# Performance work log

Hardware: AMD Instinct MI355X
Metric: run time of the kernel (lower is better)

## Reference

```python
import jax, jax.numpy as jnp
import numpy as np

B, T, D = 8, 2048, 512
KQ, K = 32, 4  # DemandRouter defaults: k_query=32, k_topk=4


def setup_inputs() -> dict:
    key = jax.random.key(0)
    ks = jax.random.split(key, 9)

    def init(k, shape, fan_in):
        return (jax.random.normal(k, shape, jnp.float32) / np.sqrt(fan_in)).astype(jnp.float32)

    return dict(
        x=jax.random.normal(ks[0], (B, T, D), jnp.float32),
        # DemandRouter projections
        Wq=init(ks[1], (D, KQ), D), bq=jnp.zeros((KQ,), jnp.float32),
        Wk=init(ks[2], (D, KQ), D), bk=jnp.zeros((KQ,), jnp.float32),
        # System1 FFN (D -> 2D -> D) + LayerNorm
        W1=init(ks[3], (D, 2 * D), D), b1=jnp.zeros((2 * D,), jnp.float32),
        W2=init(ks[4], (2 * D, D), 2 * D), b2=jnp.zeros((D,), jnp.float32),
        ln_g=jnp.ones((D,), jnp.float32), ln_b=jnp.zeros((D,), jnp.float32),
        # System2 transform (2D -> 2D -> D)
        Wt1=init(ks[5], (2 * D, 2 * D), 2 * D), bt1=jnp.zeros((2 * D,), jnp.float32),
        Wt2=init(ks[6], (2 * D, D), 2 * D), bt2=jnp.zeros((D,), jnp.float32),
        # output projection
        Wo=init(ks[7], (D, D), D), bo=jnp.zeros((D,), jnp.float32),
    )


def reference(x, Wq, bq, Wk, bk, W1, b1, W2, b2, ln_g, ln_b, Wt1, bt1, Wt2, bt2, Wo, bo):
    # ---- DemandRouter: topk over query-key similarity, gather neighbors, mean ----
    q = x @ Wq + bq                      # [B,T,KQ]
    k = x @ Wk + bk                      # [B,T,KQ]
    sim = jnp.einsum('btk,bsk->bts', q, k) / np.float32(np.sqrt(KQ))  # [B,T,T]
    _, idx = jax.lax.top_k(sim, K)       # [B,T,K]
    # gather x[b, idx[b,t]] and mean over K neighbors -> [B,T,D]
    gathered = jax.vmap(lambda xb, ib: xb[ib])(x, idx).mean(axis=2)

    # ---- System1: residual FFN (exact GELU) + LayerNorm ----
    h = jax.nn.gelu(gathered @ W1 + b1, approximate=False) @ W2 + b2
    y = gathered + h
    mu = y.mean(-1, keepdims=True)
    var = y.var(-1, keepdims=True)
    y = (y - mu) / jnp.sqrt(var + 1e-5) * ln_g + ln_b  # [B,T,D]

    # ---- System2: sequential gated memory update over T ----
    def step(mem, xt):  # mem: [B,D], xt: [B,D]
        e = jnp.concatenate([xt, mem], axis=-1)                       # [B,2D]
        prop = jax.nn.gelu(e @ Wt1 + bt1, approximate=False) @ Wt2 + bt2  # [B,D]
        g = jax.nn.sigmoid(prop)
        mem = mem * (1.0 - g) + prop * g
        return mem, None

    mem0 = jnp.zeros((y.shape[0], y.shape[2]), y.dtype)
    mem_final, _ = jax.lax.scan(step, mem0, jnp.swapaxes(y, 0, 1))

    # pooled = system2_out[:, -1] == final memory
    return mem_final @ Wo + bo  # [B,D]
```

## Files before the change

kernel.cpp:

```cpp
#include <hip/hip_runtime.h>
#include <math.h>
#include <stdint.h>


using bf16x8 = __attribute__((ext_vector_type(8))) short;
using f32x4v = __attribute__((ext_vector_type(4))) float;
typedef unsigned long long ull;

__device__ inline unsigned short f2b(float f) {
  union { float f; unsigned int u; } v; v.f = f;
  unsigned int r = v.u + 0x7fffu + ((v.u >> 16) & 1u);
  return (unsigned short)(r >> 16);
}

__device__ inline float gelu_f(float x) {
  return 0.5f * x * (1.0f + erff(x * 0.70710678118654752f));
}

__device__ inline void ins4(float v, int i,
                            float& v0, int& i0, float& v1, int& i1,
                            float& v2, int& i2, float& v3, int& i3) {
  bool b0 = (v > v0) || (v == v0 && i < i0);
  bool b1 = (v > v1) || (v == v1 && i < i1);
  bool b2 = (v > v2) || (v == v2 && i < i2);
  bool b3 = (v > v3) || (v == v3 && i < i3);
  float nv3 = b2 ? v2 : (b3 ? v : v3); int ni3 = b2 ? i2 : (b3 ? i : i3);
  float nv2 = b1 ? v1 : (b2 ? v : v2); int ni2 = b1 ? i1 : (b2 ? i : i2);
  float nv1 = b0 ? v0 : (b1 ? v : v1); int ni1 = b0 ? i0 : (b1 ? i : i1);
  float nv0 = b0 ? v  : v0;            int ni0 = b0 ? i  : i0;
  v0=nv0; i0=ni0; v1=nv1; i1=ni1; v2=nv2; i2=ni2; v3=nv3; i3=ni3;
}


__global__ __launch_bounds__(256)
void wqk_kernel(const float* __restrict__ Wq, const float* __restrict__ Wk,
                float* __restrict__ wqk) {
  int id = blockIdx.x * 256 + threadIdx.x;
  int d = id >> 6, c = id & 63;
  wqk[id] = (c < 32) ? Wq[d * 32 + c] : Wk[d * 32 + (c - 32)];
}

__global__ __launch_bounds__(256)
void transpose_bf16_kernel(const float* __restrict__ src,
                           unsigned short* __restrict__ dst, int K, int N) {
  __shared__ float tile[32][33];
  int bk = blockIdx.x << 5, bn = blockIdx.y << 5;
  int c = threadIdx.x & 31, r8 = threadIdx.x >> 5;
  for (int r = r8; r < 32; r += 8) tile[r][c] = src[(size_t)(bk + r) * N + bn + c];
  __syncthreads();
  for (int r = r8; r < 32; r += 8) dst[(size_t)(bn + r) * K + bk + c] = f2b(tile[c][r]);
}

__global__ __launch_bounds__(256)
void transpose_f32_kernel(const float* __restrict__ src,
                          float* __restrict__ dst, int K, int N) {
  __shared__ float tile[32][33];
  int bk = blockIdx.x << 5, bn = blockIdx.y << 5;
  int c = threadIdx.x & 31, r8 = threadIdx.x >> 5;
  for (int r = r8; r < 32; r += 8) tile[r][c] = src[(size_t)(bk + r) * N + bn + c];
  __syncthreads();
  for (int r = r8; r < 32; r += 8) dst[(size_t)(bn + r) * K + bk + c] = tile[c][r];
}


__global__ __launch_bounds__(256)
void qk_kernel(const float* __restrict__ x, const float* __restrict__ wqk,
               const float* __restrict__ bq, const float* __restrict__ bk,
               float* __restrict__ qkout) {
  __shared__ float xs[16][512];
  int tid = threadIdx.x;
  int b = blockIdx.x >> 7;
  int t0 = (blockIdx.x & 127) << 4;
  const float* xb = x + ((size_t)(b * 2048 + t0)) * 512;
#pragma unroll
  for (int i = 0; i < 8; ++i) {
    int f = i * 256 + tid;
    int r = f >> 7, c4 = f & 127;
    *(float4*)&xs[r][c4 * 4] = *(const float4*)&xb[(size_t)r * 512 + c4 * 4];
  }
  __syncthreads();
  int c = tid & 63, r4 = tid >> 6;
  float a0 = 0.f, a1 = 0.f, a2 = 0.f, a3 = 0.f;
#pragma unroll 4
  for (int d = 0; d < 512; ++d) {
    float w = wqk[d * 64 + c];
    a0 += xs[r4][d] * w;
    a1 += xs[r4 + 4][d] * w;
    a2 += xs[r4 + 8][d] * w;
    a3 += xs[r4 + 12][d] * w;
  }
  float bias = (c < 32) ? bq[c] : bk[c - 32];
  size_t base = ((size_t)(b * 2048 + t0)) * 64 + c;
  qkout[base + (size_t)r4 * 64] = a0 + bias;
  qkout[base + (size_t)(r4 + 4) * 64] = a1 + bias;
  qkout[base + (size_t)(r4 + 8) * 64] = a2 + bias;
  qkout[base + (size_t)(r4 + 12) * 64] = a3 + bias;
}

__global__ __launch_bounds__(256)
void topk_kernel(const float* __restrict__ qkb, int* __restrict__ idxout) {
  __shared__ float qs[16][36];
  __shared__ float ks[128][36];
  __shared__ float mv[16][16][4];
  __shared__ int   mi[16][16][4];
  int tid = threadIdx.x;
  int b = blockIdx.x >> 7;
  int t0 = (blockIdx.x & 127) << 4;
  const float* qb = qkb + ((size_t)b * 2048) * 64;
  if (tid < 128) {
    int r = tid >> 3, c4 = tid & 7;
    *(float4*)&qs[r][c4 * 4] = *(const float4*)&qb[(size_t)(t0 + r) * 64 + c4 * 4];
  }
  __syncthreads();
  int tl = tid >> 4, sl = tid & 15;
  float qv[32];
#pragma unroll
  for (int kk = 0; kk < 32; ++kk) qv[kk] = qs[tl][kk];
  float v0 = -INFINITY, v1 = -INFINITY, v2 = -INFINITY, v3 = -INFINITY;
  int i0 = 0x7fffffff, i1 = 0x7fffffff, i2 = 0x7fffffff, i3 = 0x7fffffff;
  for (int s0 = 0; s0 < 2048; s0 += 128) {
    __syncthreads();
#pragma unroll
    for (int p = 0; p < 4; ++p) {
      int f = p * 256 + tid;
      int r = f >> 3, c4 = f & 7;
      *(float4*)&ks[r][c4 * 4] =
          *(const float4*)&qb[(size_t)(s0 + r) * 64 + 32 + c4 * 4];
    }
    __syncthreads();
#pragma unroll
    for (int j = 0; j < 8; ++j) {
      int srow = j * 16 + sl;
      float accv = 0.f;
#pragma unroll
      for (int k4 = 0; k4 < 8; ++k4) {
        float4 kv = *(const float4*)&ks[srow][k4 * 4];
        accv += qv[k4 * 4 + 0] * kv.x + qv[k4 * 4 + 1] * kv.y +
                qv[k4 * 4 + 2] * kv.z + qv[k4 * 4 + 3] * kv.w;
      }
      ins4(accv, s0 + srow, v0, i0, v1, i1, v2, i2, v3, i3);
    }
  }
  mv[tl][sl][0] = v0; mv[tl][sl][1] = v1; mv[tl][sl][2] = v2; mv[tl][sl][3] = v3;
  mi[tl][sl][0] = i0; mi[tl][sl][1] = i1; mi[tl][sl][2] = i2; mi[tl][sl][3] = i3;
  __syncthreads();
  if (tid < 16) {
    float w0 = -INFINITY, w1 = -INFINITY, w2 = -INFINITY, w3 = -INFINITY;
    int a0 = 0x7fffffff, a1 = 0x7fffffff, a2 = 0x7fffffff, a3 = 0x7fffffff;
    for (int ss = 0; ss < 16; ++ss)
#pragma unroll
      for (int q = 0; q < 4; ++q)
        ins4(mv[tid][ss][q], mi[tid][ss][q], w0, a0, w1, a1, w2, a2, w3, a3);
    int4 o; o.x = a0; o.y = a1; o.z = a2; o.w = a3;
    *(int4*)&idxout[((size_t)(b * 2048 + t0 + tid)) * 4] = o;
  }
}

__global__ __launch_bounds__(128)
void gather_kernel(const float* __restrict__ x, const int* __restrict__ idx,
                   float* __restrict__ gf, unsigned short* __restrict__ gb) {
  int bt = blockIdx.x;
  int b = bt >> 11;
  const int4 iv = *(const int4*)&idx[(size_t)bt * 4];
  int tid = threadIdx.x;
  const float* xb = x + ((size_t)b * 2048) * 512;
  float4 p0 = *(const float4*)&xb[(size_t)iv.x * 512 + tid * 4];
  float4 p1 = *(const float4*)&xb[(size_t)iv.y * 512 + tid * 4];
  float4 p2 = *(const float4*)&xb[(size_t)iv.z * 512 + tid * 4];
  float4 p3 = *(const float4*)&xb[(size_t)iv.w * 512 + tid * 4];
  float4 m;
  m.x = (p0.x + p1.x + p2.x + p3.x) * 0.25f;
  m.y = (p0.y + p1.y + p2.y + p3.y) * 0.25f;
  m.z = (p0.z + p1.z + p2.z + p3.z) * 0.25f;
  m.w = (p0.w + p1.w + p2.w + p3.w) * 0.25f;
  *(float4*)&gf[(size_t)bt * 512 + tid * 4] = m;
  ushort4 u; u.x = f2b(m.x); u.y = f2b(m.y); u.z = f2b(m.z); u.w = f2b(m.w);
  *(ushort4*)&gb[(size_t)bt * 512 + tid * 4] = u;
}


template <int MODE>
__global__ __launch_bounds__(256, 2)
void gemm_bf16_k(const unsigned short* __restrict__ A,
                 const unsigned short* __restrict__ Bt,
                 const float* __restrict__ bias,
                 const float* __restrict__ resid,
                 void* __restrict__ outp, int M, int N, int K) {
  __shared__ unsigned short sA[128 * 32];
  __shared__ unsigned short sB[128 * 32];
  const int tid = threadIdx.x;
  const int lane = tid & 63, wave = tid >> 6;
  const int m0 = blockIdx.x * 128, n0 = blockIdx.y * 128;
  const int col16 = lane & 15, quad = lane >> 4;
  const int wm = wave >> 1, wn = wave & 1;
  f32x4v acc[4][4];
#pragma unroll
  for (int i = 0; i < 4; ++i)
#pragma unroll
    for (int j = 0; j < 4; ++j) {
      f32x4v z = {0.f, 0.f, 0.f, 0.f};
      acc[i][j] = z;
    }
  const int nkt = K >> 5;
  for (int kt = 0; kt < nkt; ++kt) {
    const int k0 = kt << 5;
#pragma unroll
    for (int p = 0; p < 2; ++p) {
      int f = p * 256 + tid;
      int row = f >> 2, q4 = f & 3;
      *(uint4*)&sA[row * 32 + q4 * 8] =
          *(const uint4*)(A + (size_t)(m0 + row) * K + k0 + q4 * 8);
      *(uint4*)&sB[row * 32 + q4 * 8] =
          *(const uint4*)(Bt + (size_t)(n0 + row) * K + k0 + q4 * 8);
    }
    __syncthreads();
    bf16x8 af[4], bfr[4];
#pragma unroll
    for (int i = 0; i < 4; ++i)
      af[i] = *(const bf16x8*)&sA[(wm * 64 + i * 16 + col16) * 32 + quad * 8];
#pragma unroll
    for (int j = 0; j < 4; ++j)
      bfr[j] = *(const bf16x8*)&sB[(wn * 64 + j * 16 + col16) * 32 + quad * 8];
#pragma unroll
    for (int i = 0; i < 4; ++i)
#pragma unroll
      for (int j = 0; j < 4; ++j)
        acc[i][j] = __builtin_amdgcn_mfma_f32_16x16x32_bf16(af[i], bfr[j],
                                                            acc[i][j], 0, 0, 0);
    __syncthreads();
  }
  float* outf = (float*)outp;
  unsigned short* outb = (unsigned short*)outp;
#pragma unroll
  for (int i = 0; i < 4; ++i)
#pragma unroll
    for (int j = 0; j < 4; ++j) {
      int col = n0 + wn * 64 + j * 16 + col16;
      float bs = bias[col];
#pragma unroll
      for (int r = 0; r < 4; ++r) {
        int row = m0 + wm * 64 + i * 16 + quad * 4 + r;
        float v = acc[i][j][r] + bs;
        if (MODE == 0) {
          outb[(size_t)row * N + col] = f2b(gelu_f(v));
        } else if (MODE == 1) {
          outf[(size_t)row * N + col] = v + resid[(size_t)row * N + col];
        } else {
          outf[(size_t)row * N + col] = v;
        }
      }
    }
}


__global__ __launch_bounds__(128)
void ln_kernel(const float* __restrict__ ypre, const float* __restrict__ lg,
               const float* __restrict__ lb, unsigned short* __restrict__ yb) {
  int row = blockIdx.x, tid = threadIdx.x;
  float4 v = *(const float4*)&ypre[(size_t)row * 512 + tid * 4];
  float s = v.x + v.y + v.z + v.w;
  float sq = v.x * v.x + v.y * v.y + v.z * v.z + v.w * v.w;
#pragma unroll
  for (int off = 1; off < 64; off <<= 1) {
    s += __shfl_xor(s, off, 64);
    sq += __shfl_xor(sq, off, 64);
  }
  __shared__ float red[4];
  if ((tid & 63) == 0) { red[(tid >> 6) * 2] = s; red[(tid >> 6) * 2 + 1] = sq; }
  __syncthreads();
  float S = red[0] + red[2], SQ = red[1] + red[3];
  float mu = S * (1.f / 512.f);
  float var = SQ * (1.f / 512.f) - mu * mu;
  float rstd = rsqrtf(var + 1e-5f);
  float4 g4 = *(const float4*)&lg[tid * 4];
  float4 b4 = *(const float4*)&lb[tid * 4];
  ushort4 u;
  u.x = f2b((v.x - mu) * rstd * g4.x + b4.x);
  u.y = f2b((v.y - mu) * rstd * g4.y + b4.y);
  u.z = f2b((v.z - mu) * rstd * g4.z + b4.z);
  u.w = f2b((v.w - mu) * rstd * g4.w + b4.w);
  *(ushort4*)&yb[(size_t)row * 512 + tid * 4] = u;
}


__global__ __launch_bounds__(256)
void system2_kernel(const float* __restrict__ Wt1, const float* __restrict__ Wt2T,
                    const float* __restrict__ bt2, const float* __restrict__ xpart,
                    ull* __restrict__ guT, ull* __restrict__ memT,
                    float* __restrict__ memfinal) {
  __shared__ float WbT[32 * 516];
  __shared__ float W2S[16 * 1028];
  __shared__ float memS[512];
  __shared__ float guA[1024];
  __shared__ float parts1[256];
  __shared__ float red2[256];

  const int t = threadIdx.x;
  const int team = blockIdx.x & 7;
  const int g = blockIdx.x >> 3;
  const int ucol0 = g << 5;
  const int mcol0 = g << 4;

  for (int idx = t; idx < 32 * 512; idx += 256) {
    int j = idx & 31, k = idx >> 5;
    WbT[j * 516 + k] = Wt1[(size_t)(512 + k) * 1024 + ucol0 + j];
  }
  for (int idx = t; idx < 16 * 1024; idx += 256) {
    int dd = idx >> 10, u = idx & 1023;
    W2S[dd * 1028 + u] = Wt2T[(size_t)(mcol0 + dd) * 1024 + u];
  }
  memS[t] = 0.f;
  memS[t + 256] = 0.f;
  const float bt2r = (t < 16) ? bt2[mcol0 + t] : 0.f;
  __syncthreads();

  const int j = t & 31, c = t >> 5;
  const int dd = t & 15, c2 = t >> 4;
  const float* xp = xpart + (size_t)team * 2048 * 1024 + ucol0;
  float xv = (t < 32) ? xp[t] : 0.f;

  for (int s = 0; s < 2048; ++s) {
    const int par = s & 1;
    ull* gub = guT + (size_t)(par * 8 + team) * 1024;
    ull* memb = memT + (size_t)(par * 8 + team) * 512;
    const unsigned utag = (unsigned)(s + 1);
    const ull tagw = ((ull)utag) << 32;

    float xnext = (t < 32 && s < 2047) ? xp[(size_t)(s + 1) * 1024 + t] : 0.f;

    {
      const float* wrow = &WbT[j * 516 + c * 64];
      const float* mrow = &memS[c * 64];
      float p1 = 0.f;
#pragma unroll
      for (int i = 0; i < 64; i += 4) {
        float4 wv = *(const float4*)&wrow[i];
        float4 mv = *(const float4*)&mrow[i];
        p1 += wv.x * mv.x + wv.y * mv.y + wv.z * mv.z + wv.w * mv.w;
      }
      parts1[c * 32 + j] = p1;
    }
    __syncthreads();
    if (t < 32) {
      float u = xv;
#pragma unroll
      for (int cc = 0; cc < 8; ++cc) u += parts1[cc * 32 + t];
      float gv = gelu_f(u);
      union { float f; unsigned u; } uv; uv.f = gv;
      __hip_atomic_store(&gub[ucol0 + t], tagw | uv.u, __ATOMIC_RELAXED,
                         __HIP_MEMORY_SCOPE_AGENT);
    }
    asm volatile("" ::: "memory");

    {
      ull* p = &gub[t * 4];
      ull v0, v1, v2, v3;
      for (;;) {
        v0 = __hip_atomic_load(&p[0], __ATOMIC_RELAXED, __HIP_MEMORY_SCOPE_AGENT);
        v1 = __hip_atomic_load(&p[1], __ATOMIC_RELAXED, __HIP_MEMORY_SCOPE_AGENT);
        v2 = __hip_atomic_load(&p[2], __ATOMIC_RELAXED, __HIP_MEMORY_SCOPE_AGENT);
        v3 = __hip_atomic_load(&p[3], __ATOMIC_RELAXED, __HIP_MEMORY_SCOPE_AGENT);
        bool ok = ((unsigned)(v0 >> 32) == utag) & ((unsigned)(v1 >> 32) == utag) &
                  ((unsigned)(v2 >> 32) == utag) & ((unsigned)(v3 >> 32) == utag);
        if (ok) break;
        __builtin_amdgcn_s_sleep(1);
      }
      union { unsigned u; float f; } a0, a1, a2, a3;
      a0.u = (unsigned)v0; a1.u = (unsigned)v1;
      a2.u = (unsigned)v2; a3.u = (unsigned)v3;
      guA[t * 4 + 0] = a0.f;
      guA[t * 4 + 1] = a1.f;
      guA[t * 4 + 2] = a2.f;
      guA[t * 4 + 3] = a3.f;
    }
    __syncthreads();

    {
      const float* wrow = &W2S[dd * 1028 + c2 * 64];
      const float* grow = &guA[c2 * 64];
      float p2 = 0.f;
#pragma unroll
      for (int i = 0; i < 64; i += 4) {
        float4 wv = *(const float4*)&wrow[i];
        float4 gv = *(const float4*)&grow[i];
        p2 += wv.x * gv.x + wv.y * gv.y + wv.z * gv.z + wv.w * gv.w;
      }
      red2[c2 * 16 + dd] = p2;
    }
    __syncthreads();
    if (t < 16) {
      float prop = bt2r;
#pragma unroll
      for (int cc = 0; cc < 16; ++cc) prop += red2[cc * 16 + t];
      float gate = 1.f / (1.f + __expf(-prop));
      float mnew = memS[mcol0 + t] * (1.f - gate) + prop * gate;
      union { float f; unsigned u; } mv; mv.f = mnew;
      __hip_atomic_store(&memb[mcol0 + t], tagw | mv.u, __ATOMIC_RELAXED,
                         __HIP_MEMORY_SCOPE_AGENT);
    }
    asm volatile("" ::: "memory");

    {
      ull* q1 = &memb[t * 2];
      ull* q2 = &memb[t * 2 + 1];
      ull v1, v2;
      for (;;) {
        v1 = __hip_atomic_load(q1, __ATOMIC_RELAXED, __HIP_MEMORY_SCOPE_AGENT);
        v2 = __hip_atomic_load(q2, __ATOMIC_RELAXED, __HIP_MEMORY_SCOPE_AGENT);
        if ((unsigned)(v1 >> 32) == utag && (unsigned)(v2 >> 32) == utag) break;
        __builtin_amdgcn_s_sleep(1);
      }
      union { unsigned u; float f; } m1, m2;
      m1.u = (unsigned)v1; m2.u = (unsigned)v2;
      memS[t * 2] = m1.f;
      memS[t * 2 + 1] = m2.f;
    }
    xv = xnext;
    __syncthreads();
  }

  if (g == 0 && t < 128)
    *(float4*)&memfinal[(size_t)team * 512 + t * 4] = *(float4*)&memS[t * 4];
}


__global__ __launch_bounds__(256)
void out_gemv_kernel(const float* __restrict__ memf, const float* __restrict__ Wo,
                     const float* __restrict__ bo, float* __restrict__ out) {
  int gid = blockIdx.x * 256 + threadIdx.x;
  int b = gid >> 9, d = gid & 511;
  const float* mb = memf + (size_t)b * 512;
  float acc = bo[d];
#pragma unroll 8
  for (int k = 0; k < 512; ++k) acc += mb[k] * Wo[(size_t)k * 512 + d];
  out[gid] = acc;
}


extern "C" void kernel_launch(void* const* d_in, const int* in_sizes, int n_in,
                              void* d_out, int out_size, void* d_ws, size_t ws_size,
                              hipStream_t stream) {
  const float* x   = (const float*)d_in[0];
  const float* Wq  = (const float*)d_in[1];
  const float* bq  = (const float*)d_in[2];
  const float* Wk  = (const float*)d_in[3];
  const float* bk  = (const float*)d_in[4];
  const float* W1  = (const float*)d_in[5];
  const float* b1  = (const float*)d_in[6];
  const float* W2  = (const float*)d_in[7];
  const float* b2  = (const float*)d_in[8];
  const float* lng = (const float*)d_in[9];
  const float* lnb = (const float*)d_in[10];
  const float* Wt1 = (const float*)d_in[11];
  const float* bt1 = (const float*)d_in[12];
  const float* Wt2 = (const float*)d_in[13];
  const float* bt2 = (const float*)d_in[14];
  const float* Wo  = (const float*)d_in[15];
  const float* bo  = (const float*)d_in[16];
  float* out = (float*)d_out;

  char* ws = (char*)d_ws;
  size_t off = 0;
  auto alloc = [&](size_t bytes) -> void* {
    void* p = ws + off;
    off += (bytes + 255) & ~(size_t)255;
    return p;
  };
  float* qk             = (float*)alloc(8ull * 2048 * 64 * 4);
  int* idxb             = (int*)alloc(8ull * 2048 * 4 * 4);
  float* gathf          = (float*)alloc(16384ull * 512 * 4);
  unsigned short* gathb = (unsigned short*)alloc(16384ull * 512 * 2);
  unsigned short* h1b   = (unsigned short*)alloc(16384ull * 1024 * 2);
  float* ypre           = (float*)alloc(16384ull * 512 * 4);
  unsigned short* yb    = (unsigned short*)alloc(16384ull * 512 * 2);
  float* xpart          = (float*)alloc(16384ull * 1024 * 4);
  unsigned short* w1t   = (unsigned short*)alloc(1024ull * 512 * 2);
  unsigned short* w2t   = (unsigned short*)alloc(512ull * 1024 * 2);
  unsigned short* wt1t  = (unsigned short*)alloc(1024ull * 512 * 2);
  float* wt2t           = (float*)alloc(512ull * 1024 * 4);
  float* wqkb           = (float*)alloc(512ull * 64 * 4);
  ull* guT              = (ull*)alloc(2ull * 8 * 1024 * 8);
  ull* memT             = (ull*)alloc(2ull * 8 * 512 * 8);
  float* memf           = (float*)alloc(8ull * 512 * 4);
  if (off > ws_size) return;

  wqk_kernel<<<128, 256, 0, stream>>>(Wq, Wk, wqkb);
  transpose_bf16_kernel<<<dim3(16, 32), 256, 0, stream>>>(W1, w1t, 512, 1024);
  transpose_bf16_kernel<<<dim3(32, 16), 256, 0, stream>>>(W2, w2t, 1024, 512);
  transpose_bf16_kernel<<<dim3(16, 32), 256, 0, stream>>>(Wt1, wt1t, 512, 1024);
  transpose_f32_kernel<<<dim3(32, 16), 256, 0, stream>>>(Wt2, wt2t, 1024, 512);

  qk_kernel<<<1024, 256, 0, stream>>>(x, wqkb, bq, bk, qk);
  topk_kernel<<<1024, 256, 0, stream>>>(qk, idxb);
  gather_kernel<<<16384, 128, 0, stream>>>(x, idxb, gathf, gathb);

  gemm_bf16_k<0><<<dim3(128, 8), 256, 0, stream>>>(gathb, w1t, b1, nullptr, h1b,
                                                   16384, 1024, 512);
  gemm_bf16_k<1><<<dim3(128, 4), 256, 0, stream>>>(h1b, w2t, b2, gathf, ypre,
                                                   16384, 512, 1024);
  ln_kernel<<<16384, 128, 0, stream>>>(ypre, lng, lnb, yb);
  gemm_bf16_k<2><<<dim3(128, 8), 256, 0, stream>>>(yb, wt1t, bt1, nullptr, xpart,
                                                   16384, 1024, 512);

  system2_kernel<<<256, 256, 0, stream>>>(Wt1, wt2t, bt2, xpart, guT, memT,
                                          memf);
  out_gemv_kernel<<<16, 256, 0, stream>>>(memf, Wo, bo, out);
}
```

Measured before the change: 8.765 ms.

## Interleave two batch sequences per block in the System2 recurrence to hide cross-block latency

The sequential System2 scan now gives each block two batch sequences (P and Q) instead of one, which halves the grid from 256 to 128 blocks. The phases of the two sequences are staggered so that one sequence's global spin-waits overlap the other's local GEMV work. The Q memory exchange is also deferred by one step. This aims to hide inter-block flag-polling latency on the serial critical path. In exchange each block does twice the work per step and needs more shared memory, and the tag/parity handshake gets more complex.

```diff
diff --git a/kernel.cpp b/kernel.cpp
--- a/kernel.cpp
+++ b/kernel.cpp
@@ -290,14 +290,15 @@
                     float* __restrict__ memfinal) {
   __shared__ float WbT[32 * 516];
   __shared__ float W2S[16 * 1028];
-  __shared__ float memS[512];
-  __shared__ float guA[1024];
-  __shared__ float parts1[256];
-  __shared__ float red2[256];
+  __shared__ float memP[512], memQ[512];
+  __shared__ float guP[1024], guQ[1024];
+  __shared__ float parts1P[256], parts1Q[256];
+  __shared__ float red2P[256], red2Q[256];
 
   const int t = threadIdx.x;
-  const int team = blockIdx.x & 7;
-  const int g = blockIdx.x >> 3;
+  const int team = blockIdx.x & 3;
+  const int g = blockIdx.x >> 2;
+  const int seqP = team * 2, seqQ = team * 2 + 1;
   const int ucol0 = g << 5;
   const int mcol0 = g << 4;
 
@@ -309,28 +310,31 @@
     int dd = idx >> 10, u = idx & 1023;
     W2S[dd * 1028 + u] = Wt2T[(size_t)(mcol0 + dd) * 1024 + u];
   }
-  memS[t] = 0.f;
-  memS[t + 256] = 0.f;
+  memP[t] = 0.f; memP[t + 256] = 0.f;
+  memQ[t] = 0.f; memQ[t + 256] = 0.f;
   const float bt2r = (t < 16) ? bt2[mcol0 + t] : 0.f;
   __syncthreads();
 
   const int j = t & 31, c = t >> 5;
   const int dd = t & 15, c2 = t >> 4;
-  const float* xp = xpart + (size_t)team * 2048 * 1024 + ucol0;
-  float xv = (t < 32) ? xp[t] : 0.f;
+  const float* xpP = xpart + (size_t)seqP * 2048 * 1024 + ucol0;
+  const float* xpQ = xpart + (size_t)seqQ * 2048 * 1024 + ucol0;
+  float xvP = (t < 32) ? xpP[t] : 0.f;
+  float xvQ = (t < 32) ? xpQ[t] : 0.f;
 
   for (int s = 0; s < 2048; ++s) {
     const int par = s & 1;
-    ull* gub = guT + (size_t)(par * 8 + team) * 1024;
-    ull* memb = memT + (size_t)(par * 8 + team) * 512;
+    ull* gubP = guT + (size_t)(par * 8 + seqP) * 1024;
+    ull* gubQ = guT + (size_t)(par * 8 + seqQ) * 1024;
+    ull* membP = memT + (size_t)(par * 8 + seqP) * 512;
+    ull* membQ = memT + (size_t)(par * 8 + seqQ) * 512;
+    ull* membQp = memT + (size_t)(((s + 1) & 1) * 8 + seqQ) * 512;
     const unsigned utag = (unsigned)(s + 1);
     const ull tagw = ((ull)utag) << 32;
 
-    float xnext = (t < 32 && s < 2047) ? xp[(size_t)(s + 1) * 1024 + t] : 0.f;
-
     {
       const float* wrow = &WbT[j * 516 + c * 64];
-      const float* mrow = &memS[c * 64];
+      const float* mrow = &memP[c * 64];
       float p1 = 0.f;
 #pragma unroll
       for (int i = 0; i < 64; i += 4) {
@@ -338,22 +342,58 @@
         float4 mv = *(const float4*)&mrow[i];
         p1 += wv.x * mv.x + wv.y * mv.y + wv.z * mv.z + wv.w * mv.w;
       }
-      parts1[c * 32 + j] = p1;
+      parts1P[c * 32 + j] = p1;
     }
     __syncthreads();
     if (t < 32) {
-      float u = xv;
-#pragma unroll
-      for (int cc = 0; cc < 8; ++cc) u += parts1[cc * 32 + t];
-      float gv = gelu_f(u);
-      union { float f; unsigned u; } uv; uv.f = gv;
-      __hip_atomic_store(&gub[ucol0 + t], tagw | uv.u, __ATOMIC_RELAXED,
+      float u = xvP;
+#pragma unroll
+      for (int cc = 0; cc < 8; ++cc) u += parts1P[cc * 32 + t];
+      union { float f; unsigned u; } uv; uv.f = gelu_f(u);
+      __hip_atomic_store(&gubP[ucol0 + t], tagw | uv.u, __ATOMIC_RELAXED,
                          __HIP_MEMORY_SCOPE_AGENT);
     }
     asm volatile("" ::: "memory");
-
+    if (s > 0) {
+      ull* q = &membQp[t * 2];
+      const unsigned ptag = (unsigned)s;
+      ull v1, v2;
+      for (;;) {
+        v1 = __hip_atomic_load(&q[0], __ATOMIC_RELAXED, __HIP_MEMORY_SCOPE_AGENT);
+        v2 = __hip_atomic_load(&q[1], __ATOMIC_RELAXED, __HIP_MEMORY_SCOPE_AGENT);
+        if (((unsigned)(v1 >> 32) == ptag) & ((unsigned)(v2 >> 32) == ptag)) break;
+        __builtin_amdgcn_s_sleep(1);
+      }
+      union { unsigned u; float f; } m1, m2;
+      m1.u = (unsigned)v1; m2.u = (unsigned)v2;
+      memQ[t * 2] = m1.f;
+      memQ[t * 2 + 1] = m2.f;
+    }
+    __syncthreads();
     {
-      ull* p = &gub[t * 4];
+      const float* wrow = &WbT[j * 516 + c * 64];
+      const float* mrow = &memQ[c * 64];
+      float p1 = 0.f;
+#pragma unroll
+      for (int i = 0; i < 64; i += 4) {
+        float4 wv = *(const float4*)&wrow[i];
+        float4 mv = *(const float4*)&mrow[i];
+        p1 += wv.x * mv.x + wv.y * mv.y + wv.z * mv.z + wv.w * mv.w;
+      }
+      parts1Q[c * 32 + j] = p1;
+    }
+    __syncthreads();
+    if (t < 32) {
+      float u = xvQ;
+#pragma unroll
+      for (int cc = 0; cc < 8; ++cc) u += parts1Q[cc * 32 + t];
+      union { float f; unsigned u; } uv; uv.f = gelu_f(u);
+      __hip_atomic_store(&gubQ[ucol0 + t], tagw | uv.u, __ATOMIC_RELAXED,
+                         __HIP_MEMORY_SCOPE_AGENT);
+    }
+    asm volatile("" ::: "memory");
+    {
+      ull* p = &gubP[t * 4];
       ull v0, v1, v2, v3;
       for (;;) {
         v0 = __hip_atomic_load(&p[0], __ATOMIC_RELAXED, __HIP_MEMORY_SCOPE_AGENT);
@@ -368,16 +408,17 @@
       union { unsigned u; float f; } a0, a1, a2, a3;
       a0.u = (unsigned)v0; a1.u = (unsigned)v1;
       a2.u = (unsigned)v2; a3.u = (unsigned)v3;
-      guA[t * 4 + 0] = a0.f;
-      guA[t * 4 + 1] = a1.f;
-      guA[t * 4 + 2] = a2.f;
-      guA[t * 4 + 3] = a3.f;
-    }
-    __syncthreads();
-
+      guP[t * 4 + 0] = a0.f;
+      guP[t * 4 + 1] = a1.f;
+      guP[t * 4 + 2] = a2.f;
+      guP[t * 4 + 3] = a3.f;
+    }
+    float xnP = (t < 32 && s < 2047) ? xpP[(size_t)(s + 1) * 1024 + t] : 0.f;
+    float xnQ = (t < 32 && s < 2047) ? xpQ[(size_t)(s + 1) * 1024 + t] : 0.f;
+    __syncthreads();
     {
       const float* wrow = &W2S[dd * 1028 + c2 * 64];
-      const float* grow = &guA[c2 * 64];
+      const float* grow = &guP[c2 * 64];
       float p2 = 0.f;
 #pragma unroll
       for (int i = 0; i < 64; i += 4) {
@@ -385,42 +426,107 @@
         float4 gv = *(const float4*)&grow[i];
         p2 += wv.x * gv.x + wv.y * gv.y + wv.z * gv.z + wv.w * gv.w;
       }
-      red2[c2 * 16 + dd] = p2;
+      red2P[c2 * 16 + dd] = p2;
     }
     __syncthreads();
     if (t < 16) {
       float prop = bt2r;
 #pragma unroll
-      for (int cc = 0; cc < 16; ++cc) prop += red2[cc * 16 + t];
+      for (int cc = 0; cc < 16; ++cc) prop += red2P[cc * 16 + t];
       float gate = 1.f / (1.f + __expf(-prop));
-      float mnew = memS[mcol0 + t] * (1.f - gate) + prop * gate;
+      float mnew = memP[mcol0 + t] * (1.f - gate) + prop * gate;
       union { float f; unsigned u; } mv; mv.f = mnew;
-      __hip_atomic_store(&memb[mcol0 + t], tagw | mv.u, __ATOMIC_RELAXED,
+      __hip_atomic_store(&membP[mcol0 + t], tagw | mv.u, __ATOMIC_RELAXED,
                          __HIP_MEMORY_SCOPE_AGENT);
     }
     asm volatile("" ::: "memory");
-
     {
-      ull* q1 = &memb[t * 2];
-      ull* q2 = &memb[t * 2 + 1];
+      ull* p = &gubQ[t * 4];
+      ull v0, v1, v2, v3;
+      for (;;) {
+        v0 = __hip_atomic_load(&p[0], __ATOMIC_RELAXED, __HIP_MEMORY_SCOPE_AGENT);
+        v1 = __hip_atomic_load(&p[1], __ATOMIC_RELAXED, __HIP_MEMORY_SCOPE_AGENT);
+        v2 = __hip_atomic_load(&p[2], __ATOMIC_RELAXED, __HIP_MEMORY_SCOPE_AGENT);
+        v3 = __hip_atomic_load(&p[3], __ATOMIC_RELAXED, __HIP_MEMORY_SCOPE_AGENT);
+        bool ok = ((unsigned)(v0 >> 32) == utag) & ((unsigned)(v1 >> 32) == utag) &
+                  ((unsigned)(v2 >> 32) == utag) & ((unsigned)(v3 >> 32) == utag);
+        if (ok) break;
+        __builtin_amdgcn_s_sleep(1);
+      }
+      union { unsigned u; float f; } a0, a1, a2, a3;
+      a0.u = (unsigned)v0; a1.u = (unsigned)v1;
+      a2.u = (unsigned)v2; a3.u = (unsigned)v3;
+      guQ[t * 4 + 0] = a0.f;
+      guQ[t * 4 + 1] = a1.f;
+      guQ[t * 4 + 2] = a2.f;
+      guQ[t * 4 + 3] = a3.f;
+    }
+    __syncthreads();
+    {
+      const float* wrow = &W2S[dd * 1028 + c2 * 64];
+      const float* grow = &guQ[c2 * 64];
+      float p2 = 0.f;
+#pragma unroll
+      for (int i = 0; i < 64; i += 4) {
+        float4 wv = *(const float4*)&wrow[i];
+        float4 gv = *(const float4*)&grow[i];
+        p2 += wv.x * gv.x + wv.y * gv.y + wv.z * gv.z + wv.w * gv.w;
+      }
+      red2Q[c2 * 16 + dd] = p2;
+    }
+    __syncthreads();
+    if (t < 16) {
+      float prop = bt2r;
+#pragma unroll
+      for (int cc = 0; cc < 16; ++cc) prop += red2Q[cc * 16 + t];
+      float gate = 1.f / (1.f + __expf(-prop));
+      float mnew = memQ[mcol0 + t] * (1.f - gate) + prop * gate;
+      union { float f; unsigned u; } mv; mv.f = mnew;
+      __hip_atomic_store(&membQ[mcol0 + t], tagw | mv.u, __ATOMIC_RELAXED,
+                         __HIP_MEMORY_SCOPE_AGENT);
+    }
+    asm volatile("" ::: "memory");
+    {
+      ull* q = &membP[t * 2];
       ull v1, v2;
       for (;;) {
-        v1 = __hip_atomic_load(q1, __ATOMIC_RELAXED, __HIP_MEMORY_SCOPE_AGENT);
-        v2 = __hip_atomic_load(q2, __ATOMIC_RELAXED, __HIP_MEMORY_SCOPE_AGENT);
-        if ((unsigned)(v1 >> 32) == utag && (unsigned)(v2 >> 32) == utag) break;
+        v1 = __hip_atomic_load(&q[0], __ATOMIC_RELAXED, __HIP_MEMORY_SCOPE_AGENT);
+        v2 = __hip_atomic_load(&q[1], __ATOMIC_RELAXED, __HIP_MEMORY_SCOPE_AGENT);
+        if (((unsigned)(v1 >> 32) == utag) & ((unsigned)(v2 >> 32) == utag)) break;
         __builtin_amdgcn_s_sleep(1);
       }
       union { unsigned u; float f; } m1, m2;
       m1.u = (unsigned)v1; m2.u = (unsigned)v2;
-      memS[t * 2] = m1.f;
-      memS[t * 2 + 1] = m2.f;
-    }
-    xv = xnext;
-    __syncthreads();
-  }
-
-  if (g == 0 && t < 128)
-    *(float4*)&memfinal[(size_t)team * 512 + t * 4] = *(float4*)&memS[t * 4];
+      memP[t * 2] = m1.f;
+      memP[t * 2 + 1] = m2.f;
+    }
+    xvP = xnP;
+    xvQ = xnQ;
+    __syncthreads();
+  }
+
+  {
+    ull* membQf = memT + (size_t)(1 * 8 + seqQ) * 512;
+    ull* q = &membQf[t * 2];
+    const unsigned ftag = 2048u;
+    ull v1, v2;
+    for (;;) {
+      v1 = __hip_atomic_load(&q[0], __ATOMIC_RELAXED, __HIP_MEMORY_SCOPE_AGENT);
+      v2 = __hip_atomic_load(&q[1], __ATOMIC_RELAXED, __HIP_MEMORY_SCOPE_AGENT);
+      if (((unsigned)(v1 >> 32) == ftag) & ((unsigned)(v2 >> 32) == ftag)) break;
+      __builtin_amdgcn_s_sleep(1);
+    }
+    union { unsigned u; float f; } m1, m2;
+    m1.u = (unsigned)v1; m2.u = (unsigned)v2;
+    memQ[t * 2] = m1.f;
+    memQ[t * 2 + 1] = m2.f;
+  }
+  __syncthreads();
+
+  if (g == 0 && t < 128) {
+    *(float4*)&memfinal[(size_t)seqP * 512 + t * 4] = *(float4*)&memP[t * 4];
+    *(float4*)&memfinal[(size_t)seqQ * 512 + t * 4] = *(float4*)&memQ[t * 4];
+  }
 }
 
 
@@ -502,7 +608,7 @@
   gemm_bf16_k<2><<<dim3(128, 8), 256, 0, stream>>>(yb, wt1t, bt1, nullptr, xpart,
                                                    16384, 1024, 512);
 
-  system2_kernel<<<256, 256, 0, stream>>>(Wt1, wt2t, bt2, xpart, guT, memT,
+  system2_kernel<<<128, 256, 0, stream>>>(Wt1, wt2t, bt2, xpart, guT, memT,
                                           memf);
   out_gemv_kernel<<<16, 256, 0, stream>>>(memf, Wo, bo, out);
 }
```

Result: slower. 10.10 ms (+15.2%).
